# Kernel tuning notes

Measured on AMD Instinct MI355X. Metric: run time of the kernel, lower is better.

Reference implementation:

```python
import jax, jax.numpy as jnp
import numpy as np
from jax import lax

EPS = 1e-5

def _conv1d(x, w, b):
    # x: [B,C,L], w: [O,I,K], valid padding, stride 1
    y = lax.conv_general_dilated(x, w, window_strides=(1,), padding='VALID',
                                 dimension_numbers=('NCH', 'OIH', 'NCH'))
    return y + b[None, :, None]

def setup_inputs() -> dict:
    key = jax.random.key(0)
    ks = jax.random.split(key, 7)
    B, L, C = 16, 4096, 512
    x = jax.random.normal(ks[0], (B, L, C), dtype=jnp.float32)
    fan3 = 1.0 / np.sqrt(C * 3)
    fan1 = 1.0 / np.sqrt(C * 1)
    w_down = jax.random.uniform(ks[1], (C, C, 3), jnp.float32, -fan3, fan3)
    b_down = jax.random.uniform(ks[2], (C,), jnp.float32, -fan3, fan3)
    w_pad = jax.random.uniform(ks[3], (C, C, 1), jnp.float32, -fan1, fan1)
    b_pad = jax.random.uniform(ks[4], (C,), jnp.float32, -fan1, fan1)
    gamma = jnp.ones((C,), jnp.float32)
    beta = jnp.zeros((C,), jnp.float32)
    return {"x": x, "w_down": w_down, "b_down": b_down,
            "w_pad": w_pad, "b_pad": b_pad, "gamma": gamma, "beta": beta}

def reference(x, w_down, b_down, w_pad, b_pad, gamma, beta):
    # d == 2 branch of ConvLayer
    B, L, C = x.shape

    def branch(xs):  # xs: [B, L//2, C]
        xt = jnp.transpose(xs, (0, 2, 1))                 # [B,C,L/2]
        p1 = _conv1d(xt, w_down, b_down)                  # [B,C,L/2-2]
        p2 = _conv1d(xt[:, :, :2], w_pad, b_pad)          # [B,C,2]
        return jnp.concatenate([p1, p2], axis=2)          # [B,C,L/2]

    x1_p = branch(x[:, 0::2, :])
    x2_p = branch(x[:, 1::2, :])
    # interleave: even positions from x1_p, odd from x2_p
    x_p = jnp.stack([x1_p, x2_p], axis=3).reshape(B, C, L)

    # BatchNorm1d in training mode: batch stats over (batch, length)
    mean = jnp.mean(x_p, axis=(0, 2), keepdims=True)
    var = jnp.var(x_p, axis=(0, 2), keepdims=True)
    xn = (x_p - mean) * lax.rsqrt(var + EPS)
    xn = xn * gamma[None, :, None] + beta[None, :, None]

    y = jax.nn.elu(xn)                                    # dropout = identity (eval)
    y = y + jnp.transpose(x, (0, 2, 1))                   # residual [B,C,L]

    # MaxPool1d(kernel=3, stride=2, padding=1)
    yp = jnp.pad(y, ((0, 0), (0, 0), (1, 1)), constant_values=-jnp.inf)
    pooled = lax.reduce_window(yp, -jnp.inf, lax.max, (1, 1, 3), (1, 1, 2), 'VALID')
    return jnp.transpose(pooled, (0, 2, 1))               # [B, L//2, C]
```

## Files before the change

### kernel.cpp

```cpp
#include <hip/hip_runtime.h>
#include <hip/hip_bf16.h>
#include <math.h>

typedef __bf16 bf16;
typedef __bf16 bf16x8 __attribute__((ext_vector_type(8)));
typedef float floatx4 __attribute__((ext_vector_type(4)));

#define GAS __attribute__((address_space(1)))
#define LAS __attribute__((address_space(3)))

static constexpr int B_ = 16, L_ = 4096, C_ = 512;
static constexpr int M_ = B_ * L_;
static constexpr int K_ = 3 * C_;

__global__ void prep(const float* __restrict__ x, bf16* __restrict__ xb,
                     const float* __restrict__ wd, bf16* __restrict__ wr) {
    if (blockIdx.x < 16384) {
        const size_t i = ((size_t)blockIdx.x * 256 + threadIdx.x) * 8;
        floatx4 a = *(const floatx4*)(x + i);
        floatx4 b = *(const floatx4*)(x + i + 4);
        bf16x8 o;
#pragma unroll
        for (int j = 0; j < 4; ++j) { o[j] = (bf16)a[j]; o[4 + j] = (bf16)b[j]; }
        *(bf16x8*)(xb + i) = o;
    } else {
        int idx = (blockIdx.x - 16384) * 256 + threadIdx.x;
        int o   = idx / K_;
        int rem = idx - o * K_;
        int kk  = rem >> 9;
        int i   = rem & 511;
        wr[idx] = (bf16)wd[o * K_ + i * 3 + kk];
    }
}

__global__ __launch_bounds__(512, 2) void gemm_conv(
    const bf16* __restrict__ x, const bf16* __restrict__ wr,
    const float* __restrict__ bd, bf16* __restrict__ xp, float* __restrict__ sums)
{
    __shared__ bf16 As[2 * 256 * 64];
    __shared__ bf16 Bs[2 * 256 * 64];

    const int tid = threadIdx.x;
    const int u   = blockIdx.x;
    const int mb  = (u & 7) + 8 * (u >> 4);
    const int nb  = (u >> 3) & 1;
    const int m0  = mb * 256;
    const int n0  = nb * 256;

    const int wave = tid >> 6;
    const int lane = tid & 63;
    const int wm = wave & 1;
    const int wn = wave >> 1;
    const int tm = lane & 15;
    const int quad = lane >> 4;

    floatx4 acc[2][4][2][2];
#pragma unroll
    for (int a = 0; a < 2; ++a)
#pragma unroll
        for (int b = 0; b < 4; ++b)
#pragma unroll
            for (int c = 0; c < 2; ++c)
#pragma unroll
                for (int d = 0; d < 2; ++d) acc[a][b][c][d] = floatx4{0.f, 0.f, 0.f, 0.f};

    const int r0  = tid >> 3;
    const int c0s = (tid & 7) ^ (r0 & 7);

    auto stageA = [&](int t, int eta) {
        if (t >= 24) return;
        const int kk = t >> 3, i0 = (t & 7) << 6;
        bf16* dst = As + (t & 1) * 16384 + eta * 8192 + tid * 8;
        int sr0 = m0 + eta * 128 + r0 + 2 * kk;      if (sr0 > M_ - 1) sr0 = M_ - 1;
        int sr1 = m0 + eta * 128 + r0 + 64 + 2 * kk; if (sr1 > M_ - 1) sr1 = M_ - 1;
        __builtin_amdgcn_global_load_lds((const GAS void*)(x + (size_t)sr0 * C_ + i0 + c0s * 8),
                                         (LAS void*)dst, 16, 0, 0);
        __builtin_amdgcn_global_load_lds((const GAS void*)(x + (size_t)sr1 * C_ + i0 + c0s * 8),
                                         (LAS void*)(dst + 4096), 16, 0, 0);
    };
    auto stageB = [&](int t, int eta) {
        if (t >= 24) return;
        const int kk = t >> 3, i0 = (t & 7) << 6;
        bf16* dst = Bs + (t & 1) * 16384 + eta * 8192 + tid * 8;
        const bf16* s0 = wr + (size_t)(n0 + eta * 128 + r0) * K_ + kk * C_ + i0 + c0s * 8;
        __builtin_amdgcn_global_load_lds((const GAS void*)s0, (LAS void*)dst, 16, 0, 0);
        __builtin_amdgcn_global_load_lds((const GAS void*)(s0 + (size_t)64 * K_),
                                         (LAS void*)(dst + 4096), 16, 0, 0);
    };

    const int xo0 = (quad ^ (tm & 7)) << 3;
    const int xo1 = ((4 + quad) ^ (tm & 7)) << 3;

    bf16x8 af[4][2];
    bf16x8 bfr[2][2][2];

    stageA(0, 0); stageB(0, 0); stageB(0, 1); stageA(0, 1);
    stageA(1, 0); stageB(1, 1); stageA(1, 1);
    asm volatile("s_waitcnt vmcnt(6)" ::: "memory");
    asm volatile("s_barrier" ::: "memory");

#pragma unroll 2
    for (int t = 0; t < 24; ++t) {
        const bf16* Ab = As + (t & 1) * 16384;
        const bf16* Bb = Bs + (t & 1) * 16384;

#pragma unroll
        for (int mi = 0; mi < 4; ++mi) {
            const bf16* p = Ab + (wm * 64 + mi * 16 + tm) * 64;
            af[mi][0] = *(const bf16x8*)(p + xo0);
            af[mi][1] = *(const bf16x8*)(p + xo1);
        }
#pragma unroll
        for (int ni = 0; ni < 2; ++ni) {
            const bf16* p = Bb + (wn * 32 + ni * 16 + tm) * 64;
            bfr[0][ni][0] = *(const bf16x8*)(p + xo0);
            bfr[0][ni][1] = *(const bf16x8*)(p + xo1);
        }
        stageB(t + 1, 0);
        asm volatile("s_waitcnt lgkmcnt(8)" ::: "memory");
        asm volatile("s_barrier" ::: "memory");
        asm volatile("s_waitcnt lgkmcnt(0)" ::: "memory");
        __builtin_amdgcn_s_setprio(1);
#pragma unroll
        for (int kh = 0; kh < 2; ++kh)
#pragma unroll
            for (int mi = 0; mi < 4; ++mi)
#pragma unroll
                for (int ni = 0; ni < 2; ++ni)
                    acc[0][mi][0][ni] = __builtin_amdgcn_mfma_f32_16x16x32_bf16(
                        af[mi][kh], bfr[0][ni][kh], acc[0][mi][0][ni], 0, 0, 0);
        __builtin_amdgcn_s_setprio(0);
        asm volatile("s_barrier" ::: "memory");

#pragma unroll
        for (int ni = 0; ni < 2; ++ni) {
            const bf16* p = Bb + (128 + wn * 32 + ni * 16 + tm) * 64;
            bfr[1][ni][0] = *(const bf16x8*)(p + xo0);
            bfr[1][ni][1] = *(const bf16x8*)(p + xo1);
        }
        stageA(t + 2, 0);
        asm volatile("s_barrier" ::: "memory");
        asm volatile("s_waitcnt lgkmcnt(0)" ::: "memory");
        __builtin_amdgcn_s_setprio(1);
#pragma unroll
        for (int kh = 0; kh < 2; ++kh)
#pragma unroll
            for (int mi = 0; mi < 4; ++mi)
#pragma unroll
                for (int ni = 0; ni < 2; ++ni)
                    acc[0][mi][1][ni] = __builtin_amdgcn_mfma_f32_16x16x32_bf16(
                        af[mi][kh], bfr[1][ni][kh], acc[0][mi][1][ni], 0, 0, 0);
        __builtin_amdgcn_s_setprio(0);
        asm volatile("s_barrier" ::: "memory");

#pragma unroll
        for (int mi = 0; mi < 4; ++mi) {
            const bf16* p = Ab + (128 + wm * 64 + mi * 16 + tm) * 64;
            af[mi][0] = *(const bf16x8*)(p + xo0);
            af[mi][1] = *(const bf16x8*)(p + xo1);
        }
        stageB(t + 2, 1);
        asm volatile("s_barrier" ::: "memory");
        asm volatile("s_waitcnt lgkmcnt(0)" ::: "memory");
        __builtin_amdgcn_s_setprio(1);
#pragma unroll
        for (int kh = 0; kh < 2; ++kh)
#pragma unroll
            for (int mi = 0; mi < 4; ++mi)
#pragma unroll
                for (int ni = 0; ni < 2; ++ni)
                    acc[1][mi][1][ni] = __builtin_amdgcn_mfma_f32_16x16x32_bf16(
                        af[mi][kh], bfr[1][ni][kh], acc[1][mi][1][ni], 0, 0, 0);
        __builtin_amdgcn_s_setprio(0);
        asm volatile("s_barrier" ::: "memory");

        stageA(t + 2, 1);
        if (t < 22)       { asm volatile("s_waitcnt vmcnt(6)" ::: "memory"); }
        else if (t == 22) { asm volatile("s_waitcnt vmcnt(0)" ::: "memory"); }
        asm volatile("s_barrier" ::: "memory");
        __builtin_amdgcn_s_setprio(1);
#pragma unroll
        for (int kh = 0; kh < 2; ++kh)
#pragma unroll
            for (int mi = 0; mi < 4; ++mi)
#pragma unroll
                for (int ni = 0; ni < 2; ++ni)
                    acc[1][mi][0][ni] = __builtin_amdgcn_mfma_f32_16x16x32_bf16(
                        af[mi][kh], bfr[0][ni][kh], acc[1][mi][0][ni], 0, 0, 0);
        __builtin_amdgcn_s_setprio(0);
        asm volatile("s_barrier" ::: "memory");
    }

    float bias[2][2], s[2][2], q[2][2];
#pragma unroll
    for (int nh = 0; nh < 2; ++nh)
#pragma unroll
        for (int ni = 0; ni < 2; ++ni) {
            bias[nh][ni] = bd[n0 + nh * 128 + wn * 32 + ni * 16 + tm];
            s[nh][ni] = 0.f; q[nh][ni] = 0.f;
        }

#pragma unroll
    for (int mh = 0; mh < 2; ++mh)
#pragma unroll
        for (int mi = 0; mi < 4; ++mi)
#pragma unroll
            for (int r = 0; r < 4; ++r) {
                const int m = m0 + mh * 128 + wm * 64 + mi * 16 + quad * 4 + r;
                const bool valid = (m & (L_ - 1)) < L_ - 4;
                bf16* dst = xp + (size_t)m * C_ + n0 + wn * 32 + tm;
#pragma unroll
                for (int nh = 0; nh < 2; ++nh)
#pragma unroll
                    for (int ni = 0; ni < 2; ++ni) {
                        const float v = acc[mh][mi][nh][ni][r] + bias[nh][ni];
                        dst[nh * 128 + ni * 16] = (bf16)v;
                        if (valid) { s[nh][ni] += v; q[nh][ni] += v * v; }
                    }
            }
#pragma unroll
    for (int nh = 0; nh < 2; ++nh)
#pragma unroll
        for (int ni = 0; ni < 2; ++ni) {
            float sv = s[nh][ni], qv = q[nh][ni];
            sv += __shfl_xor(sv, 16); sv += __shfl_xor(sv, 32);
            qv += __shfl_xor(qv, 16); qv += __shfl_xor(qv, 32);
            if (quad == 0) {
                const int c = n0 + nh * 128 + wn * 32 + ni * 16 + tm;
                atomicAdd(&sums[c], sv);
                atomicAdd(&sums[C_ + c], qv);
            }
        }
}

__global__ void fixup(const float* __restrict__ x, const float* __restrict__ wp,
                      const float* __restrict__ bp, bf16* __restrict__ xp,
                      float* __restrict__ sums)
{
    const int b = blockIdx.x >> 2;
    const int j = blockIdx.x & 3;
    __shared__ float xrow[C_];
    for (int i = threadIdx.x; i < C_; i += 256)
        xrow[i] = x[(size_t)(b * L_ + j) * C_ + i];
    __syncthreads();
    for (int c = threadIdx.x; c < C_; c += 256) {
        const float* w = wp + (size_t)c * C_;
        float acc = 0.f;
#pragma unroll 4
        for (int i = 0; i < C_; i += 4) {
            floatx4 wv = *(const floatx4*)(w + i);
#pragma unroll
            for (int u = 0; u < 4; ++u) acc += wv[u] * xrow[i + u];
        }
        const float v = acc + bp[c];
        xp[(size_t)(b * L_ + 4092 + j) * C_ + c] = (bf16)v;
        atomicAdd(&sums[c], v);
        atomicAdd(&sums[C_ + c], v * v);
    }
}

__global__ void final_pool(const bf16* __restrict__ xp, const bf16* __restrict__ xb,
                           const float* __restrict__ sums, const float* __restrict__ gamma,
                           const float* __restrict__ beta, float* __restrict__ out)
{
    const int gid = blockIdx.x * 256 + threadIdx.x;
    const int cg = gid & 63;
    const int t  = (gid >> 6) & 2047;
    const int b  = gid >> 17;
    const int c0 = cg << 3;

    float sc[8], sh[8];
    const float invn = 1.0f / 65536.0f;
#pragma unroll
    for (int j = 0; j < 8; ++j) {
        const int c = c0 + j;
        float mean = sums[c] * invn;
        float var  = sums[C_ + c] * invn - mean * mean;
        float scale = gamma[c] * rsqrtf(var + 1e-5f);
        sc[j] = scale;
        sh[j] = beta[c] - mean * scale;
    }

    float best[8];
#pragma unroll
    for (int j = 0; j < 8; ++j) best[j] = -INFINITY;

#pragma unroll
    for (int dl = -1; dl <= 1; ++dl) {
        const int l = 2 * t + dl;
        if (l < 0) continue;
        const size_t off = (size_t)(b * L_ + l) * C_ + c0;
        bf16x8 xpv = *(const bf16x8*)(xp + off);
        bf16x8 xv  = *(const bf16x8*)(xb + off);
#pragma unroll
        for (int j = 0; j < 8; ++j) {
            float z = sc[j] * (float)xpv[j] + sh[j];
            float y = (z > 0.f) ? z : (__expf(z) - 1.f);
            y += (float)xv[j];
            best[j] = fmaxf(best[j], y);
        }
    }
    floatx4 o0, o1;
#pragma unroll
    for (int j = 0; j < 4; ++j) { o0[j] = best[j]; o1[j] = best[4 + j]; }
    *(floatx4*)(out + (size_t)gid * 8) = o0;
    *(floatx4*)(out + (size_t)gid * 8 + 4) = o1;
}

extern "C" void kernel_launch(void* const* d_in, const int* in_sizes, int n_in,
                              void* d_out, int out_size, void* d_ws, size_t ws_size,
                              hipStream_t stream)
{
    const float* x      = (const float*)d_in[0];
    const float* w_down = (const float*)d_in[1];
    const float* b_down = (const float*)d_in[2];
    const float* w_pad  = (const float*)d_in[3];
    const float* b_pad  = (const float*)d_in[4];
    const float* gamma  = (const float*)d_in[5];
    const float* beta   = (const float*)d_in[6];
    float* out = (float*)d_out;

    char* ws = (char*)d_ws;
    bf16*  xb   = (bf16*)ws;
    bf16*  xp   = (bf16*)(ws + (size_t)M_ * C_ * 2);
    bf16*  wr   = (bf16*)(ws + (size_t)M_ * C_ * 4);
    float* sums = (float*)(ws + (size_t)M_ * C_ * 4 + (size_t)C_ * K_ * 2);

    hipMemsetAsync(sums, 0, 2 * C_ * sizeof(float), stream);
    prep<<<dim3(16384 + 3072), dim3(256), 0, stream>>>(x, xb, w_down, wr);
    gemm_conv<<<dim3(512), dim3(512), 0, stream>>>(xb, wr, b_down, xp, sums);
    fixup<<<dim3(64), dim3(256), 0, stream>>>(x, w_pad, b_pad, xp, sums);
    final_pool<<<dim3(8192), dim3(256), 0, stream>>>(xp, xb, sums, gamma, beta, out);
}
```

Baseline: 401.0 us.

## Restructure GEMM main-loop prefetch schedule and fold fixup kernel into prep

```diff
diff --git a/kernel.cpp b/kernel.cpp
--- a/kernel.cpp
+++ b/kernel.cpp
@@ -14,7 +14,9 @@
 static constexpr int K_ = 3 * C_;
 
 __global__ void prep(const float* __restrict__ x, bf16* __restrict__ xb,
-                     const float* __restrict__ wd, bf16* __restrict__ wr) {
+                     const float* __restrict__ wd, bf16* __restrict__ wr,
+                     const float* __restrict__ wp, const float* __restrict__ bp,
+                     bf16* __restrict__ xp, float* __restrict__ sums) {
     if (blockIdx.x < 16384) {
         const size_t i = ((size_t)blockIdx.x * 256 + threadIdx.x) * 8;
         floatx4 a = *(const floatx4*)(x + i);
@@ -23,13 +25,35 @@
 #pragma unroll
         for (int j = 0; j < 4; ++j) { o[j] = (bf16)a[j]; o[4 + j] = (bf16)b[j]; }
         *(bf16x8*)(xb + i) = o;
-    } else {
+    } else if (blockIdx.x < 19456) {
         int idx = (blockIdx.x - 16384) * 256 + threadIdx.x;
         int o   = idx / K_;
         int rem = idx - o * K_;
         int kk  = rem >> 9;
         int i   = rem & 511;
         wr[idx] = (bf16)wd[o * K_ + i * 3 + kk];
+    } else {
+        const int bid = blockIdx.x - 19456;
+        const int b = bid >> 2;
+        const int j = bid & 3;
+        __shared__ float xrow[C_];
+        for (int i = threadIdx.x; i < C_; i += 256)
+            xrow[i] = x[(size_t)(b * L_ + j) * C_ + i];
+        __syncthreads();
+        for (int c = threadIdx.x; c < C_; c += 256) {
+            const float* w = wp + (size_t)c * C_;
+            float acc = 0.f;
+#pragma unroll 4
+            for (int i = 0; i < C_; i += 4) {
+                floatx4 wv = *(const floatx4*)(w + i);
+#pragma unroll
+                for (int u = 0; u < 4; ++u) acc += wv[u] * xrow[i + u];
+            }
+            const float v = acc + bp[c];
+            xp[(size_t)(b * L_ + 4092 + j) * C_ + c] = (bf16)v;
+            atomicAdd(&sums[c], v);
+            atomicAdd(&sums[C_ + c], v * v);
+        }
     }
 }
 
@@ -95,31 +119,31 @@
     bf16x8 bfr[2][2][2];
 
     stageA(0, 0); stageB(0, 0); stageB(0, 1); stageA(0, 1);
-    stageA(1, 0); stageB(1, 1); stageA(1, 1);
-    asm volatile("s_waitcnt vmcnt(6)" ::: "memory");
+    stageA(1, 0); stageB(1, 0); stageB(1, 1); stageA(1, 1);
+    asm volatile("s_waitcnt vmcnt(8)" ::: "memory");
     asm volatile("s_barrier" ::: "memory");
+#pragma unroll
+    for (int mi = 0; mi < 4; ++mi) {
+        const bf16* p = As + (wm * 64 + mi * 16 + tm) * 64;
+        af[mi][0] = *(const bf16x8*)(p + xo0);
+        af[mi][1] = *(const bf16x8*)(p + xo1);
+    }
+#pragma unroll
+    for (int ni = 0; ni < 2; ++ni) {
+        const bf16* p = Bs + (wn * 32 + ni * 16 + tm) * 64;
+        bfr[0][ni][0] = *(const bf16x8*)(p + xo0);
+        bfr[0][ni][1] = *(const bf16x8*)(p + xo1);
+    }
 
 #pragma unroll 2
     for (int t = 0; t < 24; ++t) {
-        const bf16* Ab = As + (t & 1) * 16384;
-        const bf16* Bb = Bs + (t & 1) * 16384;
-
-#pragma unroll
-        for (int mi = 0; mi < 4; ++mi) {
-            const bf16* p = Ab + (wm * 64 + mi * 16 + tm) * 64;
-            af[mi][0] = *(const bf16x8*)(p + xo0);
-            af[mi][1] = *(const bf16x8*)(p + xo1);
-        }
-#pragma unroll
-        for (int ni = 0; ni < 2; ++ni) {
-            const bf16* p = Bb + (wn * 32 + ni * 16 + tm) * 64;
-            bfr[0][ni][0] = *(const bf16x8*)(p + xo0);
-            bfr[0][ni][1] = *(const bf16x8*)(p + xo1);
-        }
-        stageB(t + 1, 0);
-        asm volatile("s_waitcnt lgkmcnt(8)" ::: "memory");
-        asm volatile("s_barrier" ::: "memory");
+        const bf16* Ab  = As + (t & 1) * 16384;
+        const bf16* Bb  = Bs + (t & 1) * 16384;
+        const bf16* AbN = As + ((t + 1) & 1) * 16384;
+        const bf16* BbN = Bs + ((t + 1) & 1) * 16384;
+
         asm volatile("s_waitcnt lgkmcnt(0)" ::: "memory");
+        __builtin_amdgcn_sched_barrier(0);
         __builtin_amdgcn_s_setprio(1);
 #pragma unroll
         for (int kh = 0; kh < 2; ++kh)
@@ -130,17 +154,17 @@
                     acc[0][mi][0][ni] = __builtin_amdgcn_mfma_f32_16x16x32_bf16(
                         af[mi][kh], bfr[0][ni][kh], acc[0][mi][0][ni], 0, 0, 0);
         __builtin_amdgcn_s_setprio(0);
-        asm volatile("s_barrier" ::: "memory");
-
+        __builtin_amdgcn_sched_barrier(0);
 #pragma unroll
         for (int ni = 0; ni < 2; ++ni) {
             const bf16* p = Bb + (128 + wn * 32 + ni * 16 + tm) * 64;
             bfr[1][ni][0] = *(const bf16x8*)(p + xo0);
             bfr[1][ni][1] = *(const bf16x8*)(p + xo1);
         }
-        stageA(t + 2, 0);
-        asm volatile("s_barrier" ::: "memory");
+        asm volatile("s_barrier" ::: "memory");
+
         asm volatile("s_waitcnt lgkmcnt(0)" ::: "memory");
+        __builtin_amdgcn_sched_barrier(0);
         __builtin_amdgcn_s_setprio(1);
 #pragma unroll
         for (int kh = 0; kh < 2; ++kh)
@@ -151,17 +175,19 @@
                     acc[0][mi][1][ni] = __builtin_amdgcn_mfma_f32_16x16x32_bf16(
                         af[mi][kh], bfr[1][ni][kh], acc[0][mi][1][ni], 0, 0, 0);
         __builtin_amdgcn_s_setprio(0);
-        asm volatile("s_barrier" ::: "memory");
-
+        __builtin_amdgcn_sched_barrier(0);
 #pragma unroll
         for (int mi = 0; mi < 4; ++mi) {
             const bf16* p = Ab + (128 + wm * 64 + mi * 16 + tm) * 64;
             af[mi][0] = *(const bf16x8*)(p + xo0);
             af[mi][1] = *(const bf16x8*)(p + xo1);
         }
-        stageB(t + 2, 1);
-        asm volatile("s_barrier" ::: "memory");
+        stageA(t + 2, 0);
+        stageB(t + 2, 0);
+        asm volatile("s_barrier" ::: "memory");
+
         asm volatile("s_waitcnt lgkmcnt(0)" ::: "memory");
+        __builtin_amdgcn_sched_barrier(0);
         __builtin_amdgcn_s_setprio(1);
 #pragma unroll
         for (int kh = 0; kh < 2; ++kh)
@@ -172,10 +198,11 @@
                     acc[1][mi][1][ni] = __builtin_amdgcn_mfma_f32_16x16x32_bf16(
                         af[mi][kh], bfr[1][ni][kh], acc[1][mi][1][ni], 0, 0, 0);
         __builtin_amdgcn_s_setprio(0);
+        stageB(t + 2, 1);
         asm volatile("s_barrier" ::: "memory");
 
         stageA(t + 2, 1);
-        if (t < 22)       { asm volatile("s_waitcnt vmcnt(6)" ::: "memory"); }
+        if (t < 22)       { asm volatile("s_waitcnt vmcnt(8)" ::: "memory"); }
         else if (t == 22) { asm volatile("s_waitcnt vmcnt(0)" ::: "memory"); }
         asm volatile("s_barrier" ::: "memory");
         __builtin_amdgcn_s_setprio(1);
@@ -188,6 +215,21 @@
                     acc[1][mi][0][ni] = __builtin_amdgcn_mfma_f32_16x16x32_bf16(
                         af[mi][kh], bfr[0][ni][kh], acc[1][mi][0][ni], 0, 0, 0);
         __builtin_amdgcn_s_setprio(0);
+        __builtin_amdgcn_sched_barrier(0);
+        if (t < 23) {
+#pragma unroll
+            for (int mi = 0; mi < 4; ++mi) {
+                const bf16* p = AbN + (wm * 64 + mi * 16 + tm) * 64;
+                af[mi][0] = *(const bf16x8*)(p + xo0);
+                af[mi][1] = *(const bf16x8*)(p + xo1);
+            }
+#pragma unroll
+            for (int ni = 0; ni < 2; ++ni) {
+                const bf16* p = BbN + (wn * 32 + ni * 16 + tm) * 64;
+                bfr[0][ni][0] = *(const bf16x8*)(p + xo0);
+                bfr[0][ni][1] = *(const bf16x8*)(p + xo1);
+            }
+        }
         asm volatile("s_barrier" ::: "memory");
     }
 
@@ -214,8 +256,10 @@
 #pragma unroll
                     for (int ni = 0; ni < 2; ++ni) {
                         const float v = acc[mh][mi][nh][ni][r] + bias[nh][ni];
-                        dst[nh * 128 + ni * 16] = (bf16)v;
-                        if (valid) { s[nh][ni] += v; q[nh][ni] += v * v; }
+                        if (valid) {
+                            dst[nh * 128 + ni * 16] = (bf16)v;
+                            s[nh][ni] += v; q[nh][ni] += v * v;
+                        }
                     }
             }
 #pragma unroll
@@ -231,32 +275,6 @@
                 atomicAdd(&sums[C_ + c], qv);
             }
         }
-}
-
-__global__ void fixup(const float* __restrict__ x, const float* __restrict__ wp,
-                      const float* __restrict__ bp, bf16* __restrict__ xp,
-                      float* __restrict__ sums)
-{
-    const int b = blockIdx.x >> 2;
-    const int j = blockIdx.x & 3;
-    __shared__ float xrow[C_];
-    for (int i = threadIdx.x; i < C_; i += 256)
-        xrow[i] = x[(size_t)(b * L_ + j) * C_ + i];
-    __syncthreads();
-    for (int c = threadIdx.x; c < C_; c += 256) {
-        const float* w = wp + (size_t)c * C_;
-        float acc = 0.f;
-#pragma unroll 4
-        for (int i = 0; i < C_; i += 4) {
-            floatx4 wv = *(const floatx4*)(w + i);
-#pragma unroll
-            for (int u = 0; u < 4; ++u) acc += wv[u] * xrow[i + u];
-        }
-        const float v = acc + bp[c];
-        xp[(size_t)(b * L_ + 4092 + j) * C_ + c] = (bf16)v;
-        atomicAdd(&sums[c], v);
-        atomicAdd(&sums[C_ + c], v * v);
-    }
 }
 
 __global__ void final_pool(const bf16* __restrict__ xp, const bf16* __restrict__ xb,
@@ -327,8 +345,8 @@
     float* sums = (float*)(ws + (size_t)M_ * C_ * 4 + (size_t)C_ * K_ * 2);
 
     hipMemsetAsync(sums, 0, 2 * C_ * sizeof(float), stream);
-    prep<<<dim3(16384 + 3072), dim3(256), 0, stream>>>(x, xb, w_down, wr);
+    prep<<<dim3(16384 + 3072 + 64), dim3(256), 0, stream>>>(x, xb, w_down, wr,
+                                                            w_pad, b_pad, xp, sums);
     gemm_conv<<<dim3(512), dim3(512), 0, stream>>>(xb, wr, b_down, xp, sums);
-    fixup<<<dim3(64), dim3(256), 0, stream>>>(x, w_pad, b_pad, xp, sums);
     final_pool<<<dim3(8192), dim3(256), 0, stream>>>(xp, xb, sums, gamma, beta, out);
 }
```

After: 403.3 us. Within noise of the previous version (+0.6%).
